# Kernel optimization log

Measured on AMD Instinct MI355X. Metric: run time of the kernel, lower is better.

## Reference

```python
import jax, jax.numpy as jnp
import numpy as np

T = 128          # window length -> T-1 = 127 decoder steps
DEC = 128        # decoder_num_hidden
ENC = 128        # encoder_num_hidden
B = 2048         # batch size


def setup_inputs() -> dict:
    key = jax.random.key(0)
    ks = jax.random.split(key, 10)
    s = 0.05
    return {
        "X_encoded": jax.random.normal(ks[0], (B, T - 1, ENC), dtype=jnp.float32),
        "y_prev": jax.random.normal(ks[1], (B, T - 1), dtype=jnp.float32),
        "d_n": jnp.zeros((1, B, DEC), dtype=jnp.float32),
        "c_n": jnp.zeros((1, B, DEC), dtype=jnp.float32),
        "attn_W1": jax.random.normal(ks[2], (ENC, 2 * DEC + ENC), dtype=jnp.float32) * s,
        "attn_b1": jnp.zeros((ENC,), dtype=jnp.float32),
        "attn_W2": jax.random.normal(ks[3], (1, ENC), dtype=jnp.float32) * s,
        "attn_b2": jnp.zeros((1,), dtype=jnp.float32),
        "lstm_W_ih": jax.random.normal(ks[4], (4 * DEC, 1), dtype=jnp.float32) * s,
        "lstm_W_hh": jax.random.normal(ks[5], (4 * DEC, DEC), dtype=jnp.float32) * s,
        "lstm_b_ih": jnp.zeros((4 * DEC,), dtype=jnp.float32),
        "lstm_b_hh": jnp.zeros((4 * DEC,), dtype=jnp.float32),
        "fc_W": jax.random.normal(ks[6], (1, ENC + 1), dtype=jnp.float32),  # torch: .normal_() std=1
        "fc_b": jnp.zeros((1,), dtype=jnp.float32),
        "fcf_W": jax.random.normal(ks[7], (1, DEC + ENC), dtype=jnp.float32) * s,
        "fcf_b": jnp.zeros((1,), dtype=jnp.float32),
    }


def reference(X_encoded, y_prev, d_n, c_n,
              attn_W1, attn_b1, attn_W2, attn_b2,
              lstm_W_ih, lstm_W_hh, lstm_b_ih, lstm_b_hh,
              fc_W, fc_b, fcf_W, fcf_b):
    Bn, Tm1, enc = X_encoded.shape
    dec = d_n.shape[-1]

    def step(carry, y_t):
        d, c, _ = carry  # d,c: [B, dec]
        # temporal attention over encoder states
        d_rep = jnp.broadcast_to(d[:, None, :], (Bn, Tm1, dec))
        c_rep = jnp.broadcast_to(c[:, None, :], (Bn, Tm1, dec))
        x = jnp.concatenate([d_rep, c_rep, X_encoded], axis=2)  # [B,Tm1,2*dec+enc]
        h = jnp.tanh(jnp.einsum('bti,oi->bto', x, attn_W1) + attn_b1)
        scores = jnp.einsum('bto,ko->btk', h, attn_W2)[..., 0] + attn_b2[0]  # [B,Tm1]
        beta = jax.nn.softmax(scores, axis=1)
        context = jnp.einsum('bt,bte->be', beta, X_encoded)  # [B,enc]
        # y_tilde = fc([context, y_prev_t])
        y_tilde = jnp.concatenate([context, y_t[:, None]], axis=1) @ fc_W.T + fc_b  # [B,1]
        # single LSTM step (torch gate order i,f,g,o), input_size=1
        gates = y_tilde @ lstm_W_ih.T + d @ lstm_W_hh.T + lstm_b_ih + lstm_b_hh  # [B,4*dec]
        i, f, g, o = jnp.split(gates, 4, axis=1)
        c_new = jax.nn.sigmoid(f) * c + jax.nn.sigmoid(i) * jnp.tanh(g)
        d_new = jax.nn.sigmoid(o) * jnp.tanh(c_new)
        return (d_new, c_new, context), None

    init = (d_n[0], c_n[0], jnp.zeros((Bn, enc), dtype=X_encoded.dtype))
    (d, c, context), _ = jax.lax.scan(step, init, y_prev.T)  # scan over T-1 steps

    y_pred = jnp.concatenate([d, context], axis=1) @ fcf_W.T + fcf_b  # [B,1]
    return y_pred, d[None], c[None]
```

## Files before the change

### kernel.cpp

```cpp
#include <hip/hip_runtime.h>
#include <hip/hip_bf16.h>
#include <hip/hip_fp16.h>

#define TM1 127
#define NB  2048

typedef short s16x8 __attribute__((ext_vector_type(8)));
typedef _Float16 h16x8 __attribute__((ext_vector_type(8)));
typedef _Float16 h16x2 __attribute__((ext_vector_type(2)));
typedef float f32x4 __attribute__((ext_vector_type(4)));
typedef unsigned short u16x8 __attribute__((ext_vector_type(8)));

#define K1 1.4426950408889634f
#define K2 2.8853900817779268f

#define WS_XWK   0ull
#define WS_FX    67108864ull
#define WS_GX    (WS_FX + 1048576ull)
#define WS_FRAG  (WS_GX + 1048576ull)
#define WS_PAR   (WS_FRAG + 196608ull)

#define L_XW    0
#define L_DCA   131072
#define L_EPH   139264
#define L_GT    140288
#define L_SP    144384
#define L_Y     144640
#define L_PAR   146688
#define L_RED   152096
#define L_CTX   154144
#define L_TOTAL 154160

__device__ __forceinline__ float fexp2(float x){
#if __has_builtin(__builtin_amdgcn_exp2f)
  return __builtin_amdgcn_exp2f(x);
#else
  return exp2f(x);
#endif
}
__device__ __forceinline__ float frcp(float x){
#if __has_builtin(__builtin_amdgcn_rcpf)
  return __builtin_amdgcn_rcpf(x);
#else
  return 1.0f / x;
#endif
}
__device__ __forceinline__ _Float16 hrcp(_Float16 x){
#if __has_builtin(__builtin_amdgcn_rcph)
  return __builtin_amdgcn_rcph(x);
#else
  return (_Float16)frcp((float)x);
#endif
}
#if __has_builtin(__builtin_amdgcn_fdot2)
#define FDOT2(a,b,c) __builtin_amdgcn_fdot2((a),(b),(c),false)
#else
#define FDOT2(a,b,c) fmaf((float)(a)[0],(float)(b)[0], fmaf((float)(a)[1],(float)(b)[1],(c)))
#endif
__device__ __forceinline__ unsigned short f2bf(float f){
  unsigned u = __builtin_bit_cast(unsigned, f);
  u = (u + 0x7FFFu + ((u >> 16) & 1u)) >> 16;
  return (unsigned short)u;
}
__device__ __forceinline__ unsigned short f2h(float f){
  _Float16 h = (_Float16)f;
  return __builtin_bit_cast(unsigned short, h);
}
__device__ __forceinline__ float h2f(unsigned short u){
  return (float)__builtin_bit_cast(_Float16, u);
}
#if __has_builtin(__builtin_amdgcn_update_dpp)
template<int C>
__device__ __forceinline__ float dppadd(float v){
  int t = __builtin_amdgcn_update_dpp(0, __builtin_bit_cast(int, v), C, 0xF, 0xF, true);
  return v + __builtin_bit_cast(float, t);
}
#define HAVE_DPP 1
#else
#define HAVE_DPP 0
#endif

__global__ __launch_bounds__(256) void k_xw(const float* __restrict__ X,
                                            const float* __restrict__ W1,
                                            unsigned short* __restrict__ xwk){
  extern __shared__ char smem[];
  unsigned short* A  = (unsigned short*)smem;
  unsigned short* Bt = (unsigned short*)(smem + 34816);
  const int tid = threadIdx.x;
  const int bg = blockIdx.x;
  const float* Xb = X + (size_t)bg * TM1 * 128;
  for (int idx = tid; idx < 8192; idx += 256){
    int i = idx >> 6, k2 = (idx & 63) * 2;
    float x0 = 0.f, x1 = 0.f;
    if (i < TM1){ float2 v = *(const float2*)(Xb + i*128 + k2); x0 = v.x; x1 = v.y; }
    ((unsigned*)A)[i*68 + (idx & 63)] = (unsigned)f2bf(x0) | ((unsigned)f2bf(x1) << 16);
  }
  for (int idx = tid; idx < 8192; idx += 256){
    int j = idx >> 6, k2 = (idx & 63) * 2;
    float2 v = *(const float2*)(W1 + j*384 + 256 + k2);
    ((unsigned*)Bt)[j*68 + (idx & 63)] = (unsigned)f2bf(v.x) | ((unsigned)f2bf(v.y) << 16);
  }
  __syncthreads();
  const int wv = tid >> 6, l = tid & 63;
  f32x4 acc[8][2];
#pragma unroll
  for (int mt = 0; mt < 8; ++mt)
#pragma unroll
    for (int nt = 0; nt < 2; ++nt) acc[mt][nt] = (f32x4){0.f,0.f,0.f,0.f};
#pragma unroll
  for (int kt = 0; kt < 4; ++kt){
    s16x8 bf0 = *(const s16x8*)(Bt + ((wv*2+0)*16 + (l&15))*136 + (l>>4)*8 + kt*32);
    s16x8 bf1 = *(const s16x8*)(Bt + ((wv*2+1)*16 + (l&15))*136 + (l>>4)*8 + kt*32);
#pragma unroll
    for (int mt = 0; mt < 8; ++mt){
      s16x8 af = *(const s16x8*)(A + (mt*16 + (l&15))*136 + (l>>4)*8 + kt*32);
      acc[mt][0] = __builtin_amdgcn_mfma_f32_16x16x32_bf16(af, bf0, acc[mt][0], 0,0,0);
      acc[mt][1] = __builtin_amdgcn_mfma_f32_16x16x32_bf16(af, bf1, acc[mt][1], 0,0,0);
    }
  }
  unsigned short* dst = xwk + (size_t)bg * 16384;
#pragma unroll
  for (int mt = 0; mt < 8; ++mt){
#pragma unroll
    for (int nt = 0; nt < 2; ++nt){
      int j = (wv*2+nt)*16 + (l & 15);
      int jblk = j >> 3, jr = j & 7;
#pragma unroll
      for (int r = 0; r < 4; ++r){
        int i = mt*16 + (l>>4)*4 + r;
        float ux = fminf(fmaxf(acc[mt][nt][r] * K2, -15.f), 15.f);
        dst[(jblk*128 + i)*8 + jr] = f2h(fexp2(ux));
      }
    }
  }
}

__global__ __launch_bounds__(128) void k_fxgx(const float* __restrict__ X,
                                              const float* __restrict__ fcW,
                                              const float* __restrict__ fcfW,
                                              float* __restrict__ FX,
                                              float* __restrict__ GX){
  const int bg = blockIdx.x;
  const int l = threadIdx.x & 63, wv = threadIdx.x >> 6;
  float fw0 = fcW[l], fw1 = fcW[64 + l];
  float gw0 = fcfW[128 + l], gw1 = fcfW[192 + l];
  const float* Xb = X + (size_t)bg * TM1 * 128;
  for (int i = wv; i < TM1; i += 2){
    float x0 = Xb[i*128 + l], x1 = Xb[i*128 + 64 + l];
    float p = x0*fw0 + x1*fw1;
    float g = x0*gw0 + x1*gw1;
#pragma unroll
    for (int m = 1; m < 64; m <<= 1){ p += __shfl_xor(p, m, 64); g += __shfl_xor(g, m, 64); }
    if (l == 0){ FX[bg*128 + i] = p; GX[bg*128 + i] = g; }
  }
  if (threadIdx.x == 0){ FX[bg*128 + 127] = 0.f; GX[bg*128 + 127] = 0.f; }
}

__global__ __launch_bounds__(64) void k_pack(const float* __restrict__ W1,
                                             const float* __restrict__ Whh,
                                             const float* __restrict__ W2,
                                             const float* __restrict__ b1,
                                             const float* __restrict__ bih,
                                             const float* __restrict__ bhh,
                                             const float* __restrict__ Wih,
                                             const float* __restrict__ fcW,
                                             const float* __restrict__ fcb,
                                             const float* __restrict__ fcfW,
                                             const float* __restrict__ fcfb,
                                             char* __restrict__ ws){
  const int tile = blockIdx.x, l = threadIdx.x;
  s16x8 v;
  if (tile < 64){
    int nt = tile >> 3, ct = tile & 7;
    int row = nt*16 + (l & 15);
    int kb = ct*32 + (l >> 4)*8;
#pragma unroll
    for (int r = 0; r < 8; ++r) v[r] = (short)f2bf(W1[row*384 + kb + r]);
  } else {
    int g = tile - 64; int nt = g >> 2, kt = g & 3;
    int row = nt*16 + (l & 15);
    int kb = kt*32 + (l >> 4)*8;
#pragma unroll
    for (int r = 0; r < 8; ++r) v[r] = (short)f2bf(Whh[row*128 + kb + r]);
  }
  *(s16x8*)(ws + WS_FRAG + ((size_t)tile*64 + l)*16) = v;
  if (tile == 0){
    char* par = ws + WS_PAR;
    for (int j = l; j < 128; j += 64){
      ((unsigned short*)par)[j] = f2h(-2.f * W2[j]);
      ((float*)(par + 256))[j] = b1[j] * K2;
      ((float*)(par + 4864))[j] = fcfW[j];
    }
    for (int n = l; n < 512; n += 64){
      ((float*)(par + 768))[n] = bih[n] + bhh[n];
      ((float*)(par + 2816))[n] = Wih[n];
    }
    if (l == 0){
      ((float*)(par + 5376))[0] = fcW[128];
      ((float*)(par + 5376))[1] = fcb[0];
      ((float*)(par + 5376))[2] = fcfb[0];
      ((float*)(par + 5376))[3] = 0.f;
    }
  }
}

__global__ __launch_bounds__(1024, 4) void k_main(const char* __restrict__ ws,
                                                  const float* __restrict__ dn,
                                                  const float* __restrict__ cn,
                                                  const float* __restrict__ yprev,
                                                  float* __restrict__ out){
  extern __shared__ char smem[];
  const int tid = threadIdx.x;
  const int wv = tid >> 6, l = tid & 63;
  const int bg0 = blockIdx.x * 4;
  const bool wlt8 = (wv < 8);

  {
    const u16x8* src = (const u16x8*)(ws + (size_t)bg0 * 32768);
    u16x8* dstv = (u16x8*)(smem + L_XW);
    for (int c = tid; c < 8192; c += 1024) dstv[c] = src[c];
    const f32x4* ps = (const f32x4*)(ws + WS_PAR);
    f32x4* pd = (f32x4*)(smem + L_PAR);
    for (int c = tid; c < 337; c += 1024) pd[c] = ps[c];
    float* yd = (float*)(smem + L_Y);
    if (tid < 512){
      int b = tid >> 7, tt = tid & 127;
      yd[tid] = (tt < TM1) ? yprev[(size_t)(bg0 + b)*TM1 + tt] : 0.f;
    }
    unsigned* z = (unsigned*)(smem + L_DCA);
    for (int c = tid; c < 2048; c += 1024) z[c] = 0u;
  }

  size_t t0, t1, t2;
  if (wlt8){ t0 = (size_t)wv * 8192; t1 = t0 + 4096; t2 = 65536 + (size_t)wv * 4096; }
  else { int m = wv - 8; t0 = 65536 + (size_t)(8 + m*3) * 4096; t1 = t0 + 4096; t2 = t1 + 4096; }
  const char* blob = ws + WS_FRAG;
#define LB(o) (*(const s16x8*)(blob + (o) + (size_t)l*16))
  s16x8 w00=LB(t0), w01=LB(t0+1024), w02=LB(t0+2048), w03=LB(t0+3072);
  s16x8 w10=LB(t1), w11=LB(t1+1024), w12=LB(t1+2048), w13=LB(t1+3072);
  s16x8 w20=LB(t2), w21=LB(t2+1024), w22=LB(t2+2048), w23=LB(t2+3072);
#undef LB

  const int pb = tid & 3, pj = (tid >> 2) & 127;
  float d_reg = 0.f, c_reg = 0.f;
  if (tid < 512){ d_reg = dn[(bg0+pb)*128 + pj]; c_reg = cn[(bg0+pb)*128 + pj]; }

  const int b2 = wv >> 2, r0 = (wv & 3) * 32, q = l & 15, s2 = l >> 4;
  const int i2a = r0 + q, i2b = r0 + 16 + q;
  const float fxa = ((const float*)(ws + WS_FX))[(bg0 + b2)*128 + i2a];
  const float gxa = ((const float*)(ws + WS_GX))[(bg0 + b2)*128 + i2a];
  const float fxb = ((const float*)(ws + WS_FX))[(bg0 + b2)*128 + i2b];
  const float gxb = ((const float*)(ws + WS_GX))[(bg0 + b2)*128 + i2b];
  const float mb = (i2b < TM1) ? 1.f : 0.f;
  const float sel = (l < 16) ? 1.f : 0.f;

  __syncthreads();
  unsigned short* dcA = (unsigned short*)(smem + L_DCA);
  const int wr_d = ((pj >> 5)      * 64 + ((pj >> 3) & 3) * 16 + pb) * 8 + (pj & 7);
  const int wr_c = (((pj >> 5) + 4) * 64 + ((pj >> 3) & 3) * 16 + pb) * 8 + (pj & 7);
  if (tid < 512){ dcA[wr_d] = f2bf(d_reg); dcA[wr_c] = f2bf(c_reg); }

  unsigned short* eph = (unsigned short*)(smem + L_EPH);
  unsigned short* gt16 = (unsigned short*)(smem + L_GT);
  float* red = (float*)(smem + L_RED);
  float* ctxL = (float*)(smem + L_CTX);
  const float* yL = (const float*)(smem + L_Y);
  const float* b1K  = (const float*)(smem + L_PAR + 256);
  const float* bsum = (const float*)(smem + L_PAR + 768);
  const float* wih  = (const float*)(smem + L_PAR + 2816);
  const float* fcfd = (const float*)(smem + L_PAR + 4864);
  const float* scal = (const float*)(smem + L_PAR + 5376);

  float wih0 = wih[pj], wih1 = wih[128+pj], wih2 = wih[256+pj], wih3 = wih[384+pj];
  float bs0 = bsum[pj], bs1 = bsum[128+pj], bs2 = bsum[256+pj], bs3 = bsum[384+pj];
  float sc0 = scal[0], sc1 = scal[1];
  __syncthreads();

  const int abyte = l * 16;
  const int cb = wlt8 ? 1 : 0;
  float ctxg = 0.f;

  const unsigned short* xwa = (const unsigned short*)(smem + L_XW)
                              + ((b2*16 + s2*4)*128 + i2a)*8;
  const unsigned short* epb0 = eph + b2*128 + s2*32;
  const unsigned short* w2b = (const unsigned short*)(smem + L_PAR) + s2*32;

  for (int t = 0; t < TM1; ++t){
    {
      f32x4 z = (f32x4){0.f,0.f,0.f,0.f};
      f32x4 ac0 = z, ac1 = z, ac2 = z;
      s16x8 a0, a1, a2, a3, b0, b1, b2r, b3;
      a0 = *(const s16x8*)((char*)dcA + 0*1024 + abyte);
      a1 = *(const s16x8*)((char*)dcA + 1*1024 + abyte);
      a2 = *(const s16x8*)((char*)dcA + 2*1024 + abyte);
      a3 = *(const s16x8*)((char*)dcA + 3*1024 + abyte);
      if (cb){
        b0 = *(const s16x8*)((char*)dcA + 4*1024 + abyte);
        b1 = *(const s16x8*)((char*)dcA + 5*1024 + abyte);
        b2r = *(const s16x8*)((char*)dcA + 6*1024 + abyte);
        b3 = *(const s16x8*)((char*)dcA + 7*1024 + abyte);
      } else { b0 = a0; b1 = a1; b2r = a2; b3 = a3; }
      ac0 = __builtin_amdgcn_mfma_f32_16x16x32_bf16(a0, w00, ac0, 0,0,0);
      ac0 = __builtin_amdgcn_mfma_f32_16x16x32_bf16(a1, w01, ac0, 0,0,0);
      ac0 = __builtin_amdgcn_mfma_f32_16x16x32_bf16(a2, w02, ac0, 0,0,0);
      ac0 = __builtin_amdgcn_mfma_f32_16x16x32_bf16(a3, w03, ac0, 0,0,0);
      ac2 = __builtin_amdgcn_mfma_f32_16x16x32_bf16(a0, w20, ac2, 0,0,0);
      ac2 = __builtin_amdgcn_mfma_f32_16x16x32_bf16(a1, w21, ac2, 0,0,0);
      ac2 = __builtin_amdgcn_mfma_f32_16x16x32_bf16(a2, w22, ac2, 0,0,0);
      ac2 = __builtin_amdgcn_mfma_f32_16x16x32_bf16(a3, w23, ac2, 0,0,0);
      ac1 = __builtin_amdgcn_mfma_f32_16x16x32_bf16(b0, w10, ac1, 0,0,0);
      ac1 = __builtin_amdgcn_mfma_f32_16x16x32_bf16(b1, w11, ac1, 0,0,0);
      ac1 = __builtin_amdgcn_mfma_f32_16x16x32_bf16(b2r, w12, ac1, 0,0,0);
      ac1 = __builtin_amdgcn_mfma_f32_16x16x32_bf16(b3, w13, ac1, 0,0,0);
      if (l < 16){
        if (wlt8){
          int j = wv*16 + l;
          float bb = b1K[j];
          float u0 = fminf(fmaxf((ac0[0] + ac1[0])*K2 + bb, -15.f), 15.f);
          float u1 = fminf(fmaxf((ac0[1] + ac1[1])*K2 + bb, -15.f), 15.f);
          float u2 = fminf(fmaxf((ac0[2] + ac1[2])*K2 + bb, -15.f), 15.f);
          float u3 = fminf(fmaxf((ac0[3] + ac1[3])*K2 + bb, -15.f), 15.f);
          eph[0*128 + j] = f2h(fexp2(u0));
          eph[1*128 + j] = f2h(fexp2(u1));
          eph[2*128 + j] = f2h(fexp2(u2));
          eph[3*128 + j] = f2h(fexp2(u3));
          unsigned lo = (unsigned)f2h(ac2[0]) | ((unsigned)f2h(ac2[1]) << 16);
          unsigned hi = (unsigned)f2h(ac2[2]) | ((unsigned)f2h(ac2[3]) << 16);
          *(uint2*)((char*)gt16 + j*8) = make_uint2(lo, hi);
        } else {
          int nb = (8 + (wv - 8)*3)*16 + l;
          unsigned lo, hi;
          lo = (unsigned)f2h(ac0[0]) | ((unsigned)f2h(ac0[1]) << 16);
          hi = (unsigned)f2h(ac0[2]) | ((unsigned)f2h(ac0[3]) << 16);
          *(uint2*)((char*)gt16 + nb*8) = make_uint2(lo, hi);
          lo = (unsigned)f2h(ac1[0]) | ((unsigned)f2h(ac1[1]) << 16);
          hi = (unsigned)f2h(ac1[2]) | ((unsigned)f2h(ac1[3]) << 16);
          *(uint2*)((char*)gt16 + (nb+16)*8) = make_uint2(lo, hi);
          lo = (unsigned)f2h(ac2[0]) | ((unsigned)f2h(ac2[1]) << 16);
          hi = (unsigned)f2h(ac2[2]) | ((unsigned)f2h(ac2[3]) << 16);
          *(uint2*)((char*)gt16 + (nb+32)*8) = make_uint2(lo, hi);
        }
      }
    }
    __syncthreads();

    {
      float sacc_a = 0.f, sacc_b = 0.f;
#pragma unroll
      for (int k = 0; k < 4; ++k){
        h16x8 ewa = *(const h16x8*)(xwa + k*1024);
        h16x8 ewb = *(const h16x8*)(xwa + k*1024 + 128);
        h16x8 ep = *(const h16x8*)(epb0 + k*8);
        h16x8 w2 = *(const h16x8*)(w2b + k*8);
        h16x8 Ea = ewa * ep;
        h16x8 Da = Ea + (_Float16)1.0f;
        h16x8 Eb = ewb * ep;
        h16x8 Db = Eb + (_Float16)1.0f;
        h16x2 ra0 = { hrcp(Da[0]), hrcp(Da[1]) };
        h16x2 ra1 = { hrcp(Da[2]), hrcp(Da[3]) };
        h16x2 ra2 = { hrcp(Da[4]), hrcp(Da[5]) };
        h16x2 ra3 = { hrcp(Da[6]), hrcp(Da[7]) };
        h16x2 rb0 = { hrcp(Db[0]), hrcp(Db[1]) };
        h16x2 rb1 = { hrcp(Db[2]), hrcp(Db[3]) };
        h16x2 rb2 = { hrcp(Db[4]), hrcp(Db[5]) };
        h16x2 rb3 = { hrcp(Db[6]), hrcp(Db[7]) };
        h16x2 wv0 = { w2[0], w2[1] }, wv1 = { w2[2], w2[3] };
        h16x2 wv2 = { w2[4], w2[5] }, wv3 = { w2[6], w2[7] };
        sacc_a = FDOT2(ra0, wv0, sacc_a);
        sacc_a = FDOT2(ra1, wv1, sacc_a);
        sacc_a = FDOT2(ra2, wv2, sacc_a);
        sacc_a = FDOT2(ra3, wv3, sacc_a);
        sacc_b = FDOT2(rb0, wv0, sacc_b);
        sacc_b = FDOT2(rb1, wv1, sacc_b);
        sacc_b = FDOT2(rb2, wv2, sacc_b);
        sacc_b = FDOT2(rb3, wv3, sacc_b);
      }
      float sa = sacc_a + __shfl_xor(sacc_a, 16, 64);
      sa += __shfl_xor(sa, 32, 64);
      float sb = sacc_b + __shfl_xor(sacc_b, 16, 64);
      sb += __shfl_xor(sb, 32, 64);
      float eea = fexp2(sa * K1);
      float eeb = fexp2(sb * K1) * mb;
      float ee = (eea + eeb) * sel;
      float aa = (eea * fxa + eeb * fxb) * sel;
      float gg = (eea * gxa + eeb * gxb) * sel;
#if HAVE_DPP
      ee = dppadd<0xB1>(ee);  aa = dppadd<0xB1>(aa);  gg = dppadd<0xB1>(gg);
      ee = dppadd<0x4E>(ee);  aa = dppadd<0x4E>(aa);  gg = dppadd<0x4E>(gg);
      ee = dppadd<0x124>(ee); aa = dppadd<0x124>(aa); gg = dppadd<0x124>(gg);
      ee = dppadd<0x128>(ee); aa = dppadd<0x128>(aa); gg = dppadd<0x128>(gg);
      if (l == 0) *(f32x4*)(smem + L_SP + wv*16) = (f32x4){ee, aa, gg, 0.f};
#else
#pragma unroll
      for (int m = 1; m < 16; m <<= 1){
        ee += __shfl_xor(ee, m, 64);
        aa += __shfl_xor(aa, m, 64);
        gg += __shfl_xor(gg, m, 64);
      }
      if (l == 0) *(f32x4*)(smem + L_SP + wv*16) = (f32x4){ee, aa, gg, 0.f};
#endif
    }
    __syncthreads();

    if (tid < 512){
      const f32x4* sp = (const f32x4*)(smem + L_SP) + pb*4;
      f32x4 p0 = sp[0], p1 = sp[1], p2 = sp[2], p3 = sp[3];
      float E = (p0[0]+p1[0]) + (p2[0]+p3[0]);
      float A = (p0[1]+p1[1]) + (p2[1]+p3[1]);
      float G = (p0[2]+p1[2]) + (p2[2]+p3[2]);
      float rE = frcp(E);
      float yt = yL[pb*128 + t];
      float ymv = A*rE + sc0*yt + sc1;
      ctxg = G*rE;
      float xi = h2f(gt16[tid       ]) + wih0*ymv + bs0;
      float xf = h2f(gt16[512  + tid]) + wih1*ymv + bs1;
      float xg = h2f(gt16[1024 + tid]) + wih2*ymv + bs2;
      float xo = h2f(gt16[1536 + tid]) + wih3*ymv + bs3;
      float si = frcp(1.f + fexp2(-xi*K1));
      float sf = frcp(1.f + fexp2(-xf*K1));
      float so = frcp(1.f + fexp2(-xo*K1));
      float tg = 1.f - 2.f*frcp(1.f + fexp2(xg*K2));
      c_reg = sf*c_reg + si*tg;
      float tc = 1.f - 2.f*frcp(1.f + fexp2(c_reg*K2));
      d_reg = so*tc;
      dcA[wr_d] = f2bf(d_reg);
      dcA[wr_c] = f2bf(c_reg);
    }
    __syncthreads();
  }

  if (tid < 512){
    out[2048 + (bg0 + pb)*128 + pj] = d_reg;
    out[2048 + 262144 + (bg0 + pb)*128 + pj] = c_reg;
    red[pb*128 + pj] = fcfd[pj] * d_reg;
    if (pj == 0) ctxL[pb] = ctxg;
  }
  __syncthreads();
  if (wv < 4){
    float v = red[wv*128 + l] + red[wv*128 + 64 + l];
#pragma unroll
    for (int m = 1; m < 64; m <<= 1) v += __shfl_xor(v, m, 64);
    if (l == 0) out[bg0 + wv] = v + ctxL[wv] + ((const float*)(smem + L_PAR + 5376))[2];
  }
}

extern "C" void kernel_launch(void* const* d_in, const int* in_sizes, int n_in,
                              void* d_out, int out_size, void* d_ws, size_t ws_size,
                              hipStream_t stream){
  const float* X     = (const float*)d_in[0];
  const float* yprev = (const float*)d_in[1];
  const float* dn    = (const float*)d_in[2];
  const float* cn    = (const float*)d_in[3];
  const float* W1    = (const float*)d_in[4];
  const float* b1    = (const float*)d_in[5];
  const float* W2    = (const float*)d_in[6];
  const float* Wih   = (const float*)d_in[8];
  const float* Whh   = (const float*)d_in[9];
  const float* bih   = (const float*)d_in[10];
  const float* bhh   = (const float*)d_in[11];
  const float* fcW   = (const float*)d_in[12];
  const float* fcb   = (const float*)d_in[13];
  const float* fcfW  = (const float*)d_in[14];
  const float* fcfb  = (const float*)d_in[15];
  char* ws = (char*)d_ws;
  float* out = (float*)d_out;
  (void)in_sizes; (void)n_in; (void)out_size; (void)ws_size;

  hipFuncSetAttribute(reinterpret_cast<const void*>(k_xw),
                      hipFuncAttributeMaxDynamicSharedMemorySize, 69632);
  hipFuncSetAttribute(reinterpret_cast<const void*>(k_main),
                      hipFuncAttributeMaxDynamicSharedMemorySize, L_TOTAL);

  k_xw<<<2048, 256, 69632, stream>>>(X, W1, (unsigned short*)ws);
  k_fxgx<<<2048, 128, 0, stream>>>(X, fcW, fcfW,
                                   (float*)(ws + WS_FX), (float*)(ws + WS_GX));
  k_pack<<<192, 64, 0, stream>>>(W1, Whh, W2, b1, bih, bhh, Wih,
                                 fcW, fcb, fcfW, fcfb, ws);
  k_main<<<512, 1024, L_TOTAL, stream>>>(ws, dn, cn, yprev, out);
}
```

Before: 930.6 us.

## Spread LSTM cell update across all waves with lane-pair gate split

The per-step LSTM gate computation used to run on only the first 512 threads (8 waves), leaving the other waves idle at the barrier. Each wave now contributes 32 state slots, and the lower and upper half-waves each compute two of the four gates, exchanging results with a cross-lane shuffle. The attention score loop is also reorganised into two sequential blocks to cut live registers, and the masks are folded into preloaded constants. This trades a shuffle and some divergent selects for a shorter critical path in the serial per-step phase.

```diff
diff --git a/kernel.cpp b/kernel.cpp
--- a/kernel.cpp
+++ b/kernel.cpp
@@ -241,24 +241,29 @@
   s16x8 w20=LB(t2), w21=LB(t2+1024), w22=LB(t2+2048), w23=LB(t2+3072);
 #undef LB
 
-  const int pb = tid & 3, pj = (tid >> 2) & 127;
+  const int slot = wv*32 + (l & 31);
+  const int pb = slot & 3, pj = (slot >> 2) & 127;
+  const bool owner = (l < 32);
+  const int ga = owner ? 0 : 2;
   float d_reg = 0.f, c_reg = 0.f;
-  if (tid < 512){ d_reg = dn[(bg0+pb)*128 + pj]; c_reg = cn[(bg0+pb)*128 + pj]; }
+  if (owner){ d_reg = dn[(bg0+pb)*128 + pj]; c_reg = cn[(bg0+pb)*128 + pj]; }
 
   const int b2 = wv >> 2, r0 = (wv & 3) * 32, q = l & 15, s2 = l >> 4;
   const int i2a = r0 + q, i2b = r0 + 16 + q;
-  const float fxa = ((const float*)(ws + WS_FX))[(bg0 + b2)*128 + i2a];
-  const float gxa = ((const float*)(ws + WS_GX))[(bg0 + b2)*128 + i2a];
-  const float fxb = ((const float*)(ws + WS_FX))[(bg0 + b2)*128 + i2b];
-  const float gxb = ((const float*)(ws + WS_GX))[(bg0 + b2)*128 + i2b];
-  const float mb = (i2b < TM1) ? 1.f : 0.f;
   const float sel = (l < 16) ? 1.f : 0.f;
+  const float mbv = (i2b < TM1) ? 1.f : 0.f;
+  const float ma = sel;
+  const float mb2 = mbv * sel;
+  const float fxa2 = ((const float*)(ws + WS_FX))[(bg0 + b2)*128 + i2a] * sel;
+  const float gxa2 = ((const float*)(ws + WS_GX))[(bg0 + b2)*128 + i2a] * sel;
+  const float fxbm = ((const float*)(ws + WS_FX))[(bg0 + b2)*128 + i2b] * mb2;
+  const float gxbm = ((const float*)(ws + WS_GX))[(bg0 + b2)*128 + i2b] * mb2;
 
   __syncthreads();
   unsigned short* dcA = (unsigned short*)(smem + L_DCA);
   const int wr_d = ((pj >> 5)      * 64 + ((pj >> 3) & 3) * 16 + pb) * 8 + (pj & 7);
   const int wr_c = (((pj >> 5) + 4) * 64 + ((pj >> 3) & 3) * 16 + pb) * 8 + (pj & 7);
-  if (tid < 512){ dcA[wr_d] = f2bf(d_reg); dcA[wr_c] = f2bf(c_reg); }
+  if (owner){ dcA[wr_d] = f2bf(d_reg); dcA[wr_c] = f2bf(c_reg); }
 
   unsigned short* eph = (unsigned short*)(smem + L_EPH);
   unsigned short* gt16 = (unsigned short*)(smem + L_GT);
@@ -271,8 +276,9 @@
   const float* fcfd = (const float*)(smem + L_PAR + 4864);
   const float* scal = (const float*)(smem + L_PAR + 5376);
 
-  float wih0 = wih[pj], wih1 = wih[128+pj], wih2 = wih[256+pj], wih3 = wih[384+pj];
-  float bs0 = bsum[pj], bs1 = bsum[128+pj], bs2 = bsum[256+pj], bs3 = bsum[384+pj];
+  float wa_ = wih[ga*128 + pj],      wb_ = wih[ga*128 + 128 + pj];
+  float ba_ = bsum[ga*128 + pj],     bb_ = bsum[ga*128 + 128 + pj];
+  float fd_ = fcfd[pj];
   float sc0 = scal[0], sc1 = scal[1];
   __syncthreads();
 
@@ -348,42 +354,42 @@
       float sacc_a = 0.f, sacc_b = 0.f;
 #pragma unroll
       for (int k = 0; k < 4; ++k){
-        h16x8 ewa = *(const h16x8*)(xwa + k*1024);
-        h16x8 ewb = *(const h16x8*)(xwa + k*1024 + 128);
         h16x8 ep = *(const h16x8*)(epb0 + k*8);
         h16x8 w2 = *(const h16x8*)(w2b + k*8);
-        h16x8 Ea = ewa * ep;
-        h16x8 Da = Ea + (_Float16)1.0f;
-        h16x8 Eb = ewb * ep;
-        h16x8 Db = Eb + (_Float16)1.0f;
-        h16x2 ra0 = { hrcp(Da[0]), hrcp(Da[1]) };
-        h16x2 ra1 = { hrcp(Da[2]), hrcp(Da[3]) };
-        h16x2 ra2 = { hrcp(Da[4]), hrcp(Da[5]) };
-        h16x2 ra3 = { hrcp(Da[6]), hrcp(Da[7]) };
-        h16x2 rb0 = { hrcp(Db[0]), hrcp(Db[1]) };
-        h16x2 rb1 = { hrcp(Db[2]), hrcp(Db[3]) };
-        h16x2 rb2 = { hrcp(Db[4]), hrcp(Db[5]) };
-        h16x2 rb3 = { hrcp(Db[6]), hrcp(Db[7]) };
-        h16x2 wv0 = { w2[0], w2[1] }, wv1 = { w2[2], w2[3] };
-        h16x2 wv2 = { w2[4], w2[5] }, wv3 = { w2[6], w2[7] };
-        sacc_a = FDOT2(ra0, wv0, sacc_a);
-        sacc_a = FDOT2(ra1, wv1, sacc_a);
-        sacc_a = FDOT2(ra2, wv2, sacc_a);
-        sacc_a = FDOT2(ra3, wv3, sacc_a);
-        sacc_b = FDOT2(rb0, wv0, sacc_b);
-        sacc_b = FDOT2(rb1, wv1, sacc_b);
-        sacc_b = FDOT2(rb2, wv2, sacc_b);
-        sacc_b = FDOT2(rb3, wv3, sacc_b);
+        {
+          h16x8 ew = *(const h16x8*)(xwa + k*1024);
+          h16x8 D = ew * ep + (_Float16)1.0f;
+          h16x2 r0 = { hrcp(D[0]), hrcp(D[1]) };
+          h16x2 r1 = { hrcp(D[2]), hrcp(D[3]) };
+          h16x2 r2 = { hrcp(D[4]), hrcp(D[5]) };
+          h16x2 r3 = { hrcp(D[6]), hrcp(D[7]) };
+          sacc_a = FDOT2(r0, ((h16x2){w2[0],w2[1]}), sacc_a);
+          sacc_a = FDOT2(r1, ((h16x2){w2[2],w2[3]}), sacc_a);
+          sacc_a = FDOT2(r2, ((h16x2){w2[4],w2[5]}), sacc_a);
+          sacc_a = FDOT2(r3, ((h16x2){w2[6],w2[7]}), sacc_a);
+        }
+        {
+          h16x8 ew = *(const h16x8*)(xwa + k*1024 + 128);
+          h16x8 D = ew * ep + (_Float16)1.0f;
+          h16x2 r0 = { hrcp(D[0]), hrcp(D[1]) };
+          h16x2 r1 = { hrcp(D[2]), hrcp(D[3]) };
+          h16x2 r2 = { hrcp(D[4]), hrcp(D[5]) };
+          h16x2 r3 = { hrcp(D[6]), hrcp(D[7]) };
+          sacc_b = FDOT2(r0, ((h16x2){w2[0],w2[1]}), sacc_b);
+          sacc_b = FDOT2(r1, ((h16x2){w2[2],w2[3]}), sacc_b);
+          sacc_b = FDOT2(r2, ((h16x2){w2[4],w2[5]}), sacc_b);
+          sacc_b = FDOT2(r3, ((h16x2){w2[6],w2[7]}), sacc_b);
+        }
       }
       float sa = sacc_a + __shfl_xor(sacc_a, 16, 64);
       sa += __shfl_xor(sa, 32, 64);
       float sb = sacc_b + __shfl_xor(sacc_b, 16, 64);
       sb += __shfl_xor(sb, 32, 64);
       float eea = fexp2(sa * K1);
-      float eeb = fexp2(sb * K1) * mb;
-      float ee = (eea + eeb) * sel;
-      float aa = (eea * fxa + eeb * fxb) * sel;
-      float gg = (eea * gxa + eeb * gxb) * sel;
+      float eeb = fexp2(sb * K1);
+      float ee = eea * ma + eeb * mb2;
+      float aa = eea * fxa2 + eeb * fxbm;
+      float gg = eea * gxa2 + eeb * gxbm;
 #if HAVE_DPP
       ee = dppadd<0xB1>(ee);  aa = dppadd<0xB1>(aa);  gg = dppadd<0xB1>(gg);
       ee = dppadd<0x4E>(ee);  aa = dppadd<0x4E>(aa);  gg = dppadd<0x4E>(gg);
@@ -402,7 +408,7 @@
     }
     __syncthreads();
 
-    if (tid < 512){
+    {
       const f32x4* sp = (const f32x4*)(smem + L_SP) + pb*4;
       f32x4 p0 = sp[0], p1 = sp[1], p2 = sp[2], p3 = sp[3];
       float E = (p0[0]+p1[0]) + (p2[0]+p3[0]);
@@ -412,27 +418,29 @@
       float yt = yL[pb*128 + t];
       float ymv = A*rE + sc0*yt + sc1;
       ctxg = G*rE;
-      float xi = h2f(gt16[tid       ]) + wih0*ymv + bs0;
-      float xf = h2f(gt16[512  + tid]) + wih1*ymv + bs1;
-      float xg = h2f(gt16[1024 + tid]) + wih2*ymv + bs2;
-      float xo = h2f(gt16[1536 + tid]) + wih3*ymv + bs3;
-      float si = frcp(1.f + fexp2(-xi*K1));
-      float sf = frcp(1.f + fexp2(-xf*K1));
-      float so = frcp(1.f + fexp2(-xo*K1));
-      float tg = 1.f - 2.f*frcp(1.f + fexp2(xg*K2));
-      c_reg = sf*c_reg + si*tg;
-      float tc = 1.f - 2.f*frcp(1.f + fexp2(c_reg*K2));
-      d_reg = so*tc;
-      dcA[wr_d] = f2bf(d_reg);
-      dcA[wr_c] = f2bf(c_reg);
+      float xa = h2f(gt16[ga*512 + slot])       + wa_*ymv + ba_;
+      float xb = h2f(gt16[ga*512 + 512 + slot]) + wb_*ymv + bb_;
+      float u1 = owner ? (-xa*K1) : (xa*K2);
+      float r1 = frcp(1.f + fexp2(u1));
+      float va = owner ? r1 : (1.f - 2.f*r1);
+      float vb = frcp(1.f + fexp2(-xb*K1));
+      float pva = __shfl_xor(va, 32, 64);
+      float pvb = __shfl_xor(vb, 32, 64);
+      if (owner){
+        c_reg = vb*c_reg + va*pva;
+        float tc = 1.f - 2.f*frcp(1.f + fexp2(c_reg*K2));
+        d_reg = pvb*tc;
+        dcA[wr_d] = f2bf(d_reg);
+        dcA[wr_c] = f2bf(c_reg);
+      }
     }
     __syncthreads();
   }
 
-  if (tid < 512){
+  if (owner){
     out[2048 + (bg0 + pb)*128 + pj] = d_reg;
     out[2048 + 262144 + (bg0 + pb)*128 + pj] = c_reg;
-    red[pb*128 + pj] = fcfd[pj] * d_reg;
+    red[pb*128 + pj] = fd_ * d_reg;
     if (pj == 0) ctxL[pb] = ctxg;
   }
   __syncthreads();
```

New measurement: 962.7 us. 1.03x slower.
